# Kernel optimization log

Hardware: AMD Instinct MI355X
Metric: run time of the kernel (lower is better)

## Reference

```python
import jax, jax.numpy as jnp
import numpy as np
from jax import lax

B, N, M = 2, 16384, 4096
C1, C2 = 128, 256
H1, H2 = 256, 128  # mlp = [C1+C2, 256, 128]


def setup_inputs() -> dict:
    key = jax.random.key(0)
    ks = jax.random.split(key, 8)
    return {
        "unknown": jax.random.normal(ks[0], (B, N, 3), jnp.float32),
        "known": jax.random.normal(ks[1], (B, M, 3), jnp.float32),
        "unknow_feats": jax.random.normal(ks[2], (B, C1, N), jnp.float32),
        "known_feats": jax.random.normal(ks[3], (B, C2, M), jnp.float32),
        "W1": jax.random.normal(ks[4], (H1, C1 + C2), jnp.float32) * 0.05,
        "b1": jnp.zeros((H1,), jnp.float32),
        "W2": jax.random.normal(ks[5], (H2, H1), jnp.float32) * 0.05,
        "b2": jnp.zeros((H2,), jnp.float32),
    }


def reference(unknown, known, unknow_feats, known_feats, W1, b1, W2, b2):
    # Pairwise squared distances (B, n, m) via ||a||^2 + ||b||^2 - 2 a.b
    d2 = (
        jnp.sum(unknown * unknown, -1)[:, :, None]
        + jnp.sum(known * known, -1)[:, None, :]
        - 2.0 * jnp.einsum("bnd,bmd->bnm", unknown, known)
    )
    # 3 nearest neighbors
    neg_d2, idx = lax.top_k(-d2, 3)  # (B, n, 3)
    dist = jnp.sqrt(jnp.maximum(-neg_d2, 0.0))  # pointops returns sqrt distances
    dist_recip = 1.0 / (dist + 1e-8)
    weight = dist_recip / jnp.sum(dist_recip, axis=2, keepdims=True)  # (B, n, 3)
    # Gather neighbor features (B, C2, n, 3) and inverse-distance weighted sum
    gathered = jax.vmap(lambda f, i: f[:, i])(known_feats, idx)
    interpolated = jnp.sum(gathered * weight[:, None, :, :], axis=-1)  # (B, C2, n)
    new_features = jnp.concatenate([interpolated, unknow_feats], axis=1)  # (B, C1+C2, n)
    # Shared MLP (1x1 convs, bn=False -> conv bias + ReLU)
    h = jax.nn.relu(jnp.einsum("oc,bcn->bon", W1, new_features) + b1[None, :, None])
    out = jax.nn.relu(jnp.einsum("oc,bcn->bon", W2, h) + b2[None, :, None])
    return out  # (B, mlp[-1], n)
```

## Files before the change

### kernel.cpp

```cpp
#include <hip/hip_runtime.h>
#include <hip/hip_bf16.h>

#define BB 2
#define NN 16384
#define MM 4096
#define C1 128
#define C2 256
#define CIN 384
#define H1 256
#define H2 128
#define PT 32

typedef __attribute__((ext_vector_type(8))) short bf16x8;
typedef __attribute__((ext_vector_type(4))) float f32x4;

__device__ __forceinline__ short f32_to_bf16(float x) {
    unsigned u = __float_as_uint(x);
    u += 0x7fffu + ((u >> 16) & 1u);
    return (short)(u >> 16);
}
__device__ __forceinline__ unsigned pack_bf16x2(float a, float b) {
    __hip_bfloat162 h = __float22bfloat162_rn(make_float2(a, b));
    union { __hip_bfloat162 h; unsigned u; } cv;
    cv.h = h;
    return cv.u;
}

__global__ __launch_bounds__(256) void prep_kernel(
    const float* __restrict__ W1, const float* __restrict__ W2,
    const float* __restrict__ known,
    short* __restrict__ W1b, short* __restrict__ W2b,
    float4* __restrict__ kpk)
{
    int i = blockIdx.x * 256 + threadIdx.x;
    if (i < H1 * CIN) W1b[i] = f32_to_bf16(W1[i]);
    if (i < H2 * H1)  W2b[i] = f32_to_bf16(W2[i]);
    if (i < BB * MM) {
        float x = known[3 * i + 0], y = known[3 * i + 1], z = known[3 * i + 2];
        kpk[i] = make_float4(x, y, z, fmaf(x, x, fmaf(y, y, z * z)));
    }
}

__global__ __launch_bounds__(1024) void knn3_kernel(
    const float* __restrict__ unknown,
    const float4* __restrict__ kpk,
    int*   __restrict__ idx_out,
    float* __restrict__ w_out)
{
    __shared__ float pdv[16][64][3];
    __shared__ float vf[64];
    __shared__ float msc[64][8];
    __shared__ int   mid[64][8];
    __shared__ int   cnt[64];

    const int b    = blockIdx.y;
    const int tid  = threadIdx.x;
    const int lane = tid & 63;
    const int wv   = __builtin_amdgcn_readfirstlane(tid >> 6);
    const int n    = blockIdx.x * 64 + lane;

    if (tid < 64) cnt[tid] = 0;

    const float ux = unknown[((size_t)b * NN + n) * 3 + 0];
    const float uy = unknown[((size_t)b * NN + n) * 3 + 1];
    const float uz = unknown[((size_t)b * NN + n) * 3 + 2];
    const float ax = -2.f * ux, ay = -2.f * uy, az = -2.f * uz;
    const float un = fmaf(ux, ux, fmaf(uy, uy, uz * uz));

    const int mbase = wv * 256;
    const float4* __restrict__ kp = kpk + (size_t)b * MM + mbase;

    float v0 = 3e38f, v1 = 3e38f, v2 = 3e38f;
    for (int m = 0; m < 256; m += 8) {
        #pragma unroll
        for (int u = 0; u < 8; ++u) {
            const float4 k = kp[m + u];
            float sc = fmaf(ax, k.x, fmaf(ay, k.y, fmaf(az, k.z, k.w)));
            v2 = __builtin_amdgcn_fmed3f(v1, sc, v2);
            v1 = __builtin_amdgcn_fmed3f(v0, sc, v1);
            v0 = fminf(sc, v0);
        }
    }
    pdv[wv][lane][0] = v0; pdv[wv][lane][1] = v1; pdv[wv][lane][2] = v2;
    __syncthreads();

    if (tid < 64) {
        float r0 = 3e38f, r1 = 3e38f, r2 = 3e38f;
        #pragma unroll
        for (int ww = 0; ww < 16; ++ww) {
            #pragma unroll
            for (int k = 0; k < 3; ++k) {
                float d = pdv[ww][tid][k];
                r2 = __builtin_amdgcn_fmed3f(r1, d, r2);
                r1 = __builtin_amdgcn_fmed3f(r0, d, r1);
                r0 = fminf(d, r0);
            }
        }
        vf[tid] = r2;
    }
    __syncthreads();

    const float v2f = vf[lane];
    for (int m = 0; m < 256; m += 8) {
        #pragma unroll
        for (int u = 0; u < 8; ++u) {
            const float4 k = kp[m + u];
            float sc = fmaf(ax, k.x, fmaf(ay, k.y, fmaf(az, k.z, k.w)));
            if (sc <= v2f) {
                int c = atomicAdd(&cnt[lane], 1);
                if (c < 8) { msc[lane][c] = sc; mid[lane][c] = mbase + m + u; }
            }
        }
    }
    __syncthreads();

    if (tid < 64) {
        const int c = cnt[tid] < 8 ? cnt[tid] : 8;
        float r0 = 3e38f, r1 = 3e38f, r2 = 3e38f;
        int   q0 = 0x7FFFFFFF, q1 = 0x7FFFFFFF, q2 = 0x7FFFFFFF;
        #pragma unroll
        for (int k = 0; k < 8; ++k) {
            float d = (k < c) ? msc[tid][k] : 3e38f;
            int   j = (k < c) ? mid[tid][k] : 0x7FFFFFFF;
            const bool lt0 = (d < r0) || (d == r0 && j < q0);
            const bool lt1 = (d < r1) || (d == r1 && j < q1);
            const bool lt2 = (d < r2) || (d == r2 && j < q2);
            float nr2 = lt1 ? r1 : (lt2 ? d : r2);
            int   nq2 = lt1 ? q1 : (lt2 ? j : q2);
            float nr1 = lt0 ? r0 : (lt1 ? d : r1);
            int   nq1 = lt0 ? q0 : (lt1 ? j : q1);
            float nr0 = lt0 ? d : r0;
            int   nq0 = lt0 ? j : q0;
            r0 = nr0; r1 = nr1; r2 = nr2; q0 = nq0; q1 = nq1; q2 = nq2;
        }
        float d0 = sqrtf(fmaxf(r0 + un, 0.f));
        float d1 = sqrtf(fmaxf(r1 + un, 0.f));
        float d2 = sqrtf(fmaxf(r2 + un, 0.f));
        float i0 = 1.f / (d0 + 1e-8f);
        float i1 = 1.f / (d1 + 1e-8f);
        float i2 = 1.f / (d2 + 1e-8f);
        float s  = i0 + i1 + i2;
        const size_t ob = ((size_t)b * NN + n) * 3;
        idx_out[ob + 0] = q0; idx_out[ob + 1] = q1; idx_out[ob + 2] = q2;
        w_out[ob + 0] = i0 / s; w_out[ob + 1] = i1 / s; w_out[ob + 2] = i2 / s;
    }
}

__global__ __launch_bounds__(256) void transpose_kernel(
    const float* __restrict__ KF, float* __restrict__ KT)
{
    __shared__ float tl[32][33];
    const int b  = blockIdx.z;
    const int m0 = blockIdx.x * 32;
    const int c0 = blockIdx.y * 32;
    const int tx = threadIdx.x & 31;
    const int ty = threadIdx.x >> 5;
    #pragma unroll
    for (int r = 0; r < 4; ++r) {
        int c = ty + r * 8;
        tl[c][tx] = KF[((size_t)b * C2 + c0 + c) * MM + m0 + tx];
    }
    __syncthreads();
    #pragma unroll
    for (int r = 0; r < 4; ++r) {
        int m = ty + r * 8;
        KT[((size_t)b * MM + m0 + m) * C2 + c0 + tx] = tl[tx][m];
    }
}

__global__ __launch_bounds__(256, 3) void fp_mlp_mfma_kernel(
    const float* __restrict__ unknow_feats,
    const float* __restrict__ KT,
    const short* __restrict__ W1b,
    const float* __restrict__ b1,
    const short* __restrict__ W2b,
    const float* __restrict__ b2,
    const int*   __restrict__ idx,
    const float* __restrict__ wgt,
    float* __restrict__ out)
{
    #define XROW 392
    #define HROW 264
    __shared__ short Xs[PT][XROW];
    __shared__ short Hs[PT][HROW];
    __shared__ int   Is[PT * 3];
    __shared__ float Ws[PT * 3];

    const int tid  = threadIdx.x;
    const int blocks_per_b = NN / PT;
    const int b    = blockIdx.x / blocks_per_b;
    const int n0   = (blockIdx.x % blocks_per_b) * PT;
    const int w    = tid >> 6;
    const int lane = tid & 63;
    const int lr   = lane & 15;
    const int lq   = lane >> 4;

    if (tid < PT * 3) {
        const size_t base = ((size_t)b * NN + n0) * 3;
        Is[tid] = idx[base + tid];
        Ws[tid] = wgt[base + tid];
    }
    __syncthreads();

    {
        const float* KTb = KT + (size_t)b * MM * C2;
        const int c4 = (lane << 2);
        #pragma unroll
        for (int pp = 0; pp < PT; pp += 4) {
            const int p = pp + w;
            const int   i0 = Is[3 * p + 0], i1 = Is[3 * p + 1], i2 = Is[3 * p + 2];
            const float w0 = Ws[3 * p + 0], w1 = Ws[3 * p + 1], w2 = Ws[3 * p + 2];
            const float4 A = *(const float4*)(KTb + (size_t)i0 * C2 + c4);
            const float4 Bv = *(const float4*)(KTb + (size_t)i1 * C2 + c4);
            const float4 Cv = *(const float4*)(KTb + (size_t)i2 * C2 + c4);
            float vx = fmaf(w0, A.x, fmaf(w1, Bv.x, w2 * Cv.x));
            float vy = fmaf(w0, A.y, fmaf(w1, Bv.y, w2 * Cv.y));
            float vz = fmaf(w0, A.z, fmaf(w1, Bv.z, w2 * Cv.z));
            float vw = fmaf(w0, A.w, fmaf(w1, Bv.w, w2 * Cv.w));
            uint2 pk;
            pk.x = pack_bf16x2(vx, vy);
            pk.y = pack_bf16x2(vz, vw);
            *(uint2*)&Xs[p][c4] = pk;
        }
        const float* UFb = unknow_feats + (size_t)b * C1 * NN + n0;
        #pragma unroll
        for (int i = 0; i < 4; ++i) {
            int e  = i * 256 + tid;
            int cc = e >> 3;
            int nq = (e & 7) << 2;
            const float4 f = *(const float4*)(UFb + (size_t)cc * NN + nq);
            Xs[nq + 0][C2 + cc] = f32_to_bf16(f.x);
            Xs[nq + 1][C2 + cc] = f32_to_bf16(f.y);
            Xs[nq + 2][C2 + cc] = f32_to_bf16(f.z);
            Xs[nq + 3][C2 + cc] = f32_to_bf16(f.w);
        }
    }
    __syncthreads();

    {
        f32x4 acc[4][2];
        #pragma unroll
        for (int t = 0; t < 4; ++t)
            #pragma unroll
            for (int p = 0; p < 2; ++p) acc[t][p] = (f32x4){0.f, 0.f, 0.f, 0.f};

        for (int k0 = 0; k0 < CIN; k0 += 32) {
            bf16x8 a[4], x[2];
            #pragma unroll
            for (int t = 0; t < 4; ++t)
                a[t] = *(const bf16x8*)(W1b + (size_t)(w * 64 + t * 16 + lr) * CIN + k0 + lq * 8);
            #pragma unroll
            for (int p = 0; p < 2; ++p)
                x[p] = *(bf16x8*)&Xs[p * 16 + lr][k0 + lq * 8];
            #pragma unroll
            for (int t = 0; t < 4; ++t)
                #pragma unroll
                for (int p = 0; p < 2; ++p)
                    acc[t][p] = __builtin_amdgcn_mfma_f32_16x16x32_bf16(a[t], x[p], acc[t][p], 0, 0, 0);
        }
        #pragma unroll
        for (int t = 0; t < 4; ++t) {
            const int obase = w * 64 + t * 16 + lq * 4;
            float bb0 = b1[obase + 0], bb1 = b1[obase + 1],
                  bb2 = b1[obase + 2], bb3 = b1[obase + 3];
            #pragma unroll
            for (int p = 0; p < 2; ++p) {
                uint2 pk;
                pk.x = pack_bf16x2(fmaxf(acc[t][p].x + bb0, 0.f),
                                   fmaxf(acc[t][p].y + bb1, 0.f));
                pk.y = pack_bf16x2(fmaxf(acc[t][p].z + bb2, 0.f),
                                   fmaxf(acc[t][p].w + bb3, 0.f));
                *(uint2*)&Hs[p * 16 + lr][obase] = pk;
            }
        }
    }
    __syncthreads();

    {
        f32x4 acc[2][2];
        #pragma unroll
        for (int t = 0; t < 2; ++t)
            #pragma unroll
            for (int p = 0; p < 2; ++p) acc[t][p] = (f32x4){0.f, 0.f, 0.f, 0.f};

        for (int k0 = 0; k0 < H1; k0 += 32) {
            bf16x8 a[2], h[2];
            #pragma unroll
            for (int t = 0; t < 2; ++t)
                a[t] = *(const bf16x8*)(W2b + (size_t)(w * 32 + t * 16 + lr) * H1 + k0 + lq * 8);
            #pragma unroll
            for (int p = 0; p < 2; ++p)
                h[p] = *(bf16x8*)&Hs[p * 16 + lr][k0 + lq * 8];
            #pragma unroll
            for (int t = 0; t < 2; ++t)
                #pragma unroll
                for (int p = 0; p < 2; ++p)
                    acc[t][p] = __builtin_amdgcn_mfma_f32_16x16x32_bf16(a[t], h[p], acc[t][p], 0, 0, 0);
        }
        #pragma unroll
        for (int t = 0; t < 2; ++t) {
            const int obase = w * 32 + t * 16 + lq * 4;
            #pragma unroll
            for (int p = 0; p < 2; ++p) {
                const int n = n0 + p * 16 + lr;
                #pragma unroll
                for (int r = 0; r < 4; ++r) {
                    const int o = obase + r;
                    out[((size_t)b * H2 + o) * NN + n] =
                        fmaxf(((const float*)&acc[t][p])[r] + b2[o], 0.f);
                }
            }
        }
    }
    #undef XROW
    #undef HROW
}

extern "C" void kernel_launch(void* const* d_in, const int* in_sizes, int n_in,
                              void* d_out, int out_size, void* d_ws, size_t ws_size,
                              hipStream_t stream) {
    const float* unknown      = (const float*)d_in[0];
    const float* known        = (const float*)d_in[1];
    const float* unknow_feats = (const float*)d_in[2];
    const float* known_feats  = (const float*)d_in[3];
    const float* W1           = (const float*)d_in[4];
    const float* b1           = (const float*)d_in[5];
    const float* W2           = (const float*)d_in[6];
    const float* b2           = (const float*)d_in[7];
    float* out = (float*)d_out;

    char* ws = (char*)d_ws;
    int*    idx = (int*)(ws);
    float*  wgt = (float*)(ws + 393216);
    short*  W1b = (short*)(ws + 786432);
    short*  W2b = (short*)(ws + 983040);
    float4* kpk = (float4*)(ws + 1048576);
    float*  KT  = (float*)(ws + 1179648);

    prep_kernel<<<(H1 * CIN + 255) / 256, 256, 0, stream>>>(W1, W2, known, W1b, W2b, kpk);

    dim3 gK(NN / 64, BB);
    knn3_kernel<<<gK, 1024, 0, stream>>>(unknown, kpk, idx, wgt);

    dim3 gT(MM / 32, C2 / 32, BB);
    transpose_kernel<<<gT, 256, 0, stream>>>(known_feats, KT);

    fp_mlp_mfma_kernel<<<BB * (NN / PT), 256, 0, stream>>>(
        unknow_feats, KT, W1b, b1, W2b, b2, idx, wgt, out);
}
```

Before: 187.1 us.

## Pack known points in SoA pairs for packed-FMA KNN and merge prep with transpose

Known-point coordinates are repacked into groups of two points laid out as xx/yy/zz/nn, so the KNN scan computes two scores per iteration with packed two-wide FMAs and a single 32-byte load. The known-feature transpose is folded into the prep kernel, removing one launch. Unroll pragmas are added to the MLP k-loops. The aim is to cut VALU instruction count in the distance scan and launch overhead, at the cost of extra shuffle work and a more complex prep kernel.

```diff
diff --git a/kernel.cpp b/kernel.cpp
--- a/kernel.cpp
+++ b/kernel.cpp
@@ -13,6 +13,8 @@
 
 typedef __attribute__((ext_vector_type(8))) short bf16x8;
 typedef __attribute__((ext_vector_type(4))) float f32x4;
+typedef __attribute__((ext_vector_type(2))) float f32x2;
+typedef __attribute__((ext_vector_type(8))) float f32x8;
 
 __device__ __forceinline__ short f32_to_bf16(float x) {
     unsigned u = __float_as_uint(x);
@@ -26,24 +28,49 @@
     return cv.u;
 }
 
-__global__ __launch_bounds__(256) void prep_kernel(
+__global__ __launch_bounds__(256) void prep_transpose_kernel(
+    const float* __restrict__ KF, float* __restrict__ KT,
     const float* __restrict__ W1, const float* __restrict__ W2,
     const float* __restrict__ known,
     short* __restrict__ W1b, short* __restrict__ W2b,
-    float4* __restrict__ kpk)
+    float* __restrict__ kpk8)
 {
-    int i = blockIdx.x * 256 + threadIdx.x;
-    if (i < H1 * CIN) W1b[i] = f32_to_bf16(W1[i]);
-    if (i < H2 * H1)  W2b[i] = f32_to_bf16(W2[i]);
-    if (i < BB * MM) {
-        float x = known[3 * i + 0], y = known[3 * i + 1], z = known[3 * i + 2];
-        kpk[i] = make_float4(x, y, z, fmaf(x, x, fmaf(y, y, z * z)));
+    const int bx = blockIdx.x;
+    if (bx < 2048) {
+        __shared__ float tl[32][33];
+        const int b  = bx >> 10;
+        const int c0 = ((bx >> 7) & 7) * 32;
+        const int m0 = (bx & 127) * 32;
+        const int tx = threadIdx.x & 31;
+        const int ty = threadIdx.x >> 5;
+        #pragma unroll
+        for (int r = 0; r < 4; ++r) {
+            int c = ty + r * 8;
+            tl[c][tx] = KF[((size_t)b * C2 + c0 + c) * MM + m0 + tx];
+        }
+        __syncthreads();
+        #pragma unroll
+        for (int r = 0; r < 4; ++r) {
+            int m = ty + r * 8;
+            KT[((size_t)b * MM + m0 + m) * C2 + c0 + tx] = tl[tx][m];
+        }
+    } else {
+        int i = (bx - 2048) * 256 + threadIdx.x;
+        if (i < H1 * CIN) W1b[i] = f32_to_bf16(W1[i]);
+        if (i < H2 * H1)  W2b[i] = f32_to_bf16(W2[i]);
+        if (i < BB * MM) {
+            float x = known[3 * i + 0], y = known[3 * i + 1], z = known[3 * i + 2];
+            float n = fmaf(x, x, fmaf(y, y, z * z));
+            int g = i >> 1, j = i & 1;
+            float* base = kpk8 + (size_t)g * 8;
+            base[0 + j] = x; base[2 + j] = y; base[4 + j] = z; base[6 + j] = n;
+        }
     }
 }
 
 __global__ __launch_bounds__(1024) void knn3_kernel(
     const float* __restrict__ unknown,
-    const float4* __restrict__ kpk,
+    const float* __restrict__ kpk8,
     int*   __restrict__ idx_out,
     float* __restrict__ w_out)
 {
@@ -64,22 +91,33 @@
     const float ux = unknown[((size_t)b * NN + n) * 3 + 0];
     const float uy = unknown[((size_t)b * NN + n) * 3 + 1];
     const float uz = unknown[((size_t)b * NN + n) * 3 + 2];
-    const float ax = -2.f * ux, ay = -2.f * uy, az = -2.f * uz;
+    const f32x2 ax2 = {-2.f * ux, -2.f * ux};
+    const f32x2 ay2 = {-2.f * uy, -2.f * uy};
+    const f32x2 az2 = {-2.f * uz, -2.f * uz};
     const float un = fmaf(ux, ux, fmaf(uy, uy, uz * uz));
 
-    const int mbase = wv * 256;
-    const float4* __restrict__ kp = kpk + (size_t)b * MM + mbase;
+    const int gbase = wv * 128;
+    const float* __restrict__ kp = kpk8 + ((size_t)b * (MM / 2) + gbase) * 8;
 
     float v0 = 3e38f, v1 = 3e38f, v2 = 3e38f;
-    for (int m = 0; m < 256; m += 8) {
-        #pragma unroll
-        for (int u = 0; u < 8; ++u) {
-            const float4 k = kp[m + u];
-            float sc = fmaf(ax, k.x, fmaf(ay, k.y, fmaf(az, k.z, k.w)));
-            v2 = __builtin_amdgcn_fmed3f(v1, sc, v2);
-            v1 = __builtin_amdgcn_fmed3f(v0, sc, v1);
-            v0 = fminf(sc, v0);
-        }
+    #pragma unroll 4
+    for (int g = 0; g < 128; ++g) {
+        const f32x8 G = *(const f32x8*)(kp + (size_t)g * 8);
+        const f32x2 kx = __builtin_shufflevector(G, G, 0, 1);
+        const f32x2 ky = __builtin_shufflevector(G, G, 2, 3);
+        const f32x2 kz = __builtin_shufflevector(G, G, 4, 5);
+        const f32x2 kn = __builtin_shufflevector(G, G, 6, 7);
+        const f32x2 sc2 = __builtin_elementwise_fma(ax2, kx,
+                          __builtin_elementwise_fma(ay2, ky,
+                          __builtin_elementwise_fma(az2, kz, kn)));
+        float sa = sc2.x;
+        v2 = __builtin_amdgcn_fmed3f(v1, sa, v2);
+        v1 = __builtin_amdgcn_fmed3f(v0, sa, v1);
+        v0 = fminf(sa, v0);
+        float sb = sc2.y;
+        v2 = __builtin_amdgcn_fmed3f(v1, sb, v2);
+        v1 = __builtin_amdgcn_fmed3f(v0, sb, v1);
+        v0 = fminf(sb, v0);
     }
     pdv[wv][lane][0] = v0; pdv[wv][lane][1] = v1; pdv[wv][lane][2] = v2;
     __syncthreads();
@@ -101,14 +139,24 @@
     __syncthreads();
 
     const float v2f = vf[lane];
-    for (int m = 0; m < 256; m += 8) {
-        #pragma unroll
-        for (int u = 0; u < 8; ++u) {
-            const float4 k = kp[m + u];
-            float sc = fmaf(ax, k.x, fmaf(ay, k.y, fmaf(az, k.z, k.w)));
-            if (sc <= v2f) {
+    #pragma unroll 4
+    for (int g = 0; g < 128; ++g) {
+        const f32x8 G = *(const f32x8*)(kp + (size_t)g * 8);
+        const f32x2 kx = __builtin_shufflevector(G, G, 0, 1);
+        const f32x2 ky = __builtin_shufflevector(G, G, 2, 3);
+        const f32x2 kz = __builtin_shufflevector(G, G, 4, 5);
+        const f32x2 kn = __builtin_shufflevector(G, G, 6, 7);
+        const f32x2 sc2 = __builtin_elementwise_fma(ax2, kx,
+                          __builtin_elementwise_fma(ay2, ky,
+                          __builtin_elementwise_fma(az2, kz, kn)));
+        if (fminf(sc2.x, sc2.y) <= v2f) {
+            if (sc2.x <= v2f) {
                 int c = atomicAdd(&cnt[lane], 1);
-                if (c < 8) { msc[lane][c] = sc; mid[lane][c] = mbase + m + u; }
+                if (c < 8) { msc[lane][c] = sc2.x; mid[lane][c] = (gbase + g) * 2; }
+            }
+            if (sc2.y <= v2f) {
+                int c = atomicAdd(&cnt[lane], 1);
+                if (c < 8) { msc[lane][c] = sc2.y; mid[lane][c] = (gbase + g) * 2 + 1; }
             }
         }
     }
@@ -143,28 +191,6 @@
         const size_t ob = ((size_t)b * NN + n) * 3;
         idx_out[ob + 0] = q0; idx_out[ob + 1] = q1; idx_out[ob + 2] = q2;
         w_out[ob + 0] = i0 / s; w_out[ob + 1] = i1 / s; w_out[ob + 2] = i2 / s;
-    }
-}
-
-__global__ __launch_bounds__(256) void transpose_kernel(
-    const float* __restrict__ KF, float* __restrict__ KT)
-{
-    __shared__ float tl[32][33];
-    const int b  = blockIdx.z;
-    const int m0 = blockIdx.x * 32;
-    const int c0 = blockIdx.y * 32;
-    const int tx = threadIdx.x & 31;
-    const int ty = threadIdx.x >> 5;
-    #pragma unroll
-    for (int r = 0; r < 4; ++r) {
-        int c = ty + r * 8;
-        tl[c][tx] = KF[((size_t)b * C2 + c0 + c) * MM + m0 + tx];
-    }
-    __syncthreads();
-    #pragma unroll
-    for (int r = 0; r < 4; ++r) {
-        int m = ty + r * 8;
-        KT[((size_t)b * MM + m0 + m) * C2 + c0 + tx] = tl[tx][m];
     }
 }
 
@@ -244,6 +270,7 @@
             #pragma unroll
             for (int p = 0; p < 2; ++p) acc[t][p] = (f32x4){0.f, 0.f, 0.f, 0.f};
 
+        #pragma unroll 4
         for (int k0 = 0; k0 < CIN; k0 += 32) {
             bf16x8 a[4], x[2];
             #pragma unroll
@@ -283,6 +310,7 @@
             #pragma unroll
             for (int p = 0; p < 2; ++p) acc[t][p] = (f32x4){0.f, 0.f, 0.f, 0.f};
 
+        #pragma unroll 4
         for (int k0 = 0; k0 < H1; k0 += 32) {
             bf16x8 a[2], h[2];
             #pragma unroll
@@ -330,20 +358,18 @@
     float* out = (float*)d_out;
 
     char* ws = (char*)d_ws;
-    int*    idx = (int*)(ws);
-    float*  wgt = (float*)(ws + 393216);
-    short*  W1b = (short*)(ws + 786432);
-    short*  W2b = (short*)(ws + 983040);
-    float4* kpk = (float4*)(ws + 1048576);
-    float*  KT  = (float*)(ws + 1179648);
-
-    prep_kernel<<<(H1 * CIN + 255) / 256, 256, 0, stream>>>(W1, W2, known, W1b, W2b, kpk);
+    int*    idx  = (int*)(ws);
+    float*  wgt  = (float*)(ws + 393216);
+    short*  W1b  = (short*)(ws + 786432);
+    short*  W2b  = (short*)(ws + 983040);
+    float*  kpk8 = (float*)(ws + 1048576);
+    float*  KT   = (float*)(ws + 1179648);
+
+    prep_transpose_kernel<<<2048 + 384, 256, 0, stream>>>(
+        known_feats, KT, W1, W2, known, W1b, W2b, kpk8);
 
     dim3 gK(NN / 64, BB);
-    knn3_kernel<<<gK, 1024, 0, stream>>>(unknown, kpk, idx, wgt);
-
-    dim3 gT(MM / 32, C2 / 32, BB);
-    transpose_kernel<<<gT, 256, 0, stream>>>(known_feats, KT);
+    knn3_kernel<<<gK, 1024, 0, stream>>>(unknown, kpk8, idx, wgt);
 
     fp_mlp_mfma_kernel<<<BB * (NN / PT), 256, 0, stream>>>(
         unknow_feats, KT, W1b, b1, W2b, b2, idx, wgt, out);
```

Result: faster. 179.7 us (-3.9%).
